# Kernel tuning notes

Measured on AMD Instinct MI355X. Metric: run time of the kernel, lower is better.

## Reference

```python
import jax, jax.numpy as jnp
import numpy as np

BIG = 1e6  # sentinel 'no zero pixel found yet' distance; BIG**2 = 1e12 fits fp32


def _edt(is_fg):
    """Exact Euclidean distance transform (scipy.distance_transform_edt semantics):
    distance from each nonzero pixel to the nearest zero pixel. is_fg: [N,H,W] bool.
    Separable exact algorithm: 1D vertical distance-to-zero per column via cummax
    scans, then min-plus convolution with the parabola (j-k)^2 along rows."""
    N, H, W = is_fg.shape
    is_zero = ~is_fg
    ih = jnp.arange(H, dtype=jnp.float32)[None, :, None]
    # nearest zero at-or-above / at-or-below along H (per column)
    up = jax.lax.cummax(jnp.where(is_zero, ih, -BIG), axis=1)
    dn = -jax.lax.cummax(jnp.where(is_zero, -ih, -BIG), axis=1, reverse=True)
    g = jnp.minimum(ih - up, dn - ih)               # [N,H,W] vertical 1D distance
    g2 = jnp.minimum(g, BIG) ** 2
    ks = jnp.arange(W, dtype=jnp.float32)
    def col(j):
        # exact 2D squared distance for output column j: min_k (j-k)^2 + g(.,.,k)^2
        return jnp.min((j.astype(jnp.float32) - ks) ** 2 + g2, axis=-1)  # [N,H]
    d2 = jax.lax.map(col, jnp.arange(W))            # [W,N,H], sequential -> low memory
    return jnp.sqrt(jnp.moveaxis(d2, 0, -1))        # [N,H,W]


def setup_inputs() -> dict:
    key = jax.random.key(0)
    k1, k2 = jax.random.split(key)
    B, C, H, W = 8, 12, 256, 256
    logits = jax.random.normal(k1, (B, C, H, W), dtype=jnp.float32)
    targets = jax.random.randint(k2, (B, H, W), 0, C, dtype=jnp.int32)
    return {"logits": logits, "targets": targets}


def reference(logits, targets):
    B, C, H, W = logits.shape
    probs = jax.nn.softmax(logits, axis=1)                                  # [B,C,H,W]
    gt = targets[:, None, :, :] == jnp.arange(C, dtype=targets.dtype)[None, :, None, None]
    m = gt.reshape(B * C, H, W)
    pos = _edt(m)          # distance inside foreground to nearest background
    neg = _edt(~m)         # distance inside background to nearest foreground
    dt = (neg - pos).reshape(B, C, H, W)
    has_fg = gt.any(axis=(2, 3))                                            # [B,C]
    dt = jnp.where(has_fg[:, :, None, None], dt, 0.0)
    # per-image, per-class min-max normalization (matches torch view(B,-1).min/max)
    dmin = dt.min(axis=(2, 3), keepdims=True)
    dmax = dt.max(axis=(2, 3), keepdims=True)
    dt = (dt - dmin) / (dmax - dmin + 1e-8)
    inter = jnp.sum(probs * dt, axis=(2, 3))                                # [B,C]
    denom = jnp.sum(probs * probs, axis=(2, 3)) + jnp.sum(dt * dt, axis=(2, 3)) + 1e-6
    dice = 2.0 * inter / denom
    # sum_c mean_b (1-dice) / C  == mean over (b,c) since ignore_index=255 is out of range
    return jnp.mean(1.0 - dice)
```

## Files before the change

kernel.cpp:

```cpp
#include <hip/hip_runtime.h>
#include <math.h>

constexpr int B_  = 8;
constexpr int C_  = 12;
constexpr int H_  = 256;
constexpr int W_  = 256;
constexpr int HW_ = H_ * W_;
constexpr int NBC_ = B_ * C_;
constexpr int PAD_ = 256;
constexpr int VB_  = NBC_ * 4;
constexpr int SMB_ = B_ * (HW_ / 1024);


__global__ void __launch_bounds__(256) k_vp(
                     const int* __restrict__ t,
                     const float* __restrict__ logits,
                     unsigned short* __restrict__ gpk,
                     int* __restrict__ hasfg_p,
                     float2* __restrict__ den,
                     float* __restrict__ out) {
    int tid = threadIdx.x;
    if (blockIdx.x >= VB_) {
        int pb = blockIdx.x - VB_;
        int b = pb >> 6;
        int p = ((pb & 63) << 10) + tid * 4;
        const float* lb = logits + (size_t)b * C_ * HW_ + p;
        float4 l[C_];
        float4 mx = make_float4(-3.4e38f, -3.4e38f, -3.4e38f, -3.4e38f);
        #pragma unroll
        for (int c = 0; c < C_; ++c) {
            l[c] = *(const float4*)(lb + (size_t)c * HW_);
            mx.x = fmaxf(mx.x, l[c].x);
            mx.y = fmaxf(mx.y, l[c].y);
            mx.z = fmaxf(mx.z, l[c].z);
            mx.w = fmaxf(mx.w, l[c].w);
        }
        float4 s = make_float4(0.f, 0.f, 0.f, 0.f);
        #pragma unroll
        for (int c = 0; c < C_; ++c) {
            s.x += __expf(l[c].x - mx.x);
            s.y += __expf(l[c].y - mx.y);
            s.z += __expf(l[c].z - mx.z);
            s.w += __expf(l[c].w - mx.w);
        }
        float2* dp = den + (size_t)b * HW_ + p;
        ((float4*)dp)[0] = make_float4(mx.x, 1.0f / s.x, mx.y, 1.0f / s.y);
        ((float4*)dp)[1] = make_float4(mx.z, 1.0f / s.z, mx.w, 1.0f / s.w);
        return;
    }

    if (blockIdx.x == 0 && tid == 0) out[0] = 0.0f;
    constexpr int SEG = 8, SH = 32;
    int s  = tid >> 5;
    int wl = tid & 31;
    int blk = blockIdx.x;
    int bc = blk >> 2;
    int w0 = (blk & 3) * 64;
    int b = bc / C_, c = bc - b * C_;
    int w = w0 + 2 * wl;
    const int* base = t + b * HW_ + w;
    int h0 = s * SH;

    unsigned tp0[SH / 4], tp1[SH / 4];
    int le0 = -1, ln0 = -1, fe0 = 256, fn0 = 256;
    int le1 = -1, ln1 = -1, fe1 = 256, fn1 = 256;
    #pragma unroll
    for (int i = 0; i < SH; ++i) {
        int2 tv = *(const int2*)(base + (h0 + i) * W_);
        if ((i & 3) == 0) { tp0[i >> 2] = 0; tp1[i >> 2] = 0; }
        tp0[i >> 2] |= (unsigned)tv.x << ((i & 3) * 8);
        tp1[i >> 2] |= (unsigned)tv.y << ((i & 3) * 8);
        int h = h0 + i;
        if (tv.x == c) { le0 = h; if (fe0 == 256) fe0 = h; }
        else           { ln0 = h; if (fn0 == 256) fn0 = h; }
        if (tv.y == c) { le1 = h; if (fe1 == 256) fe1 = h; }
        else           { ln1 = h; if (fn1 == 256) fn1 = h; }
    }
    __shared__ int sLE[SEG][64], sLN[SEG][64], sFE[SEG][64], sFN[SEG][64];
    sLE[s][2 * wl] = le0; sLE[s][2 * wl + 1] = le1;
    sLN[s][2 * wl] = ln0; sLN[s][2 * wl + 1] = ln1;
    sFE[s][2 * wl] = fe0; sFE[s][2 * wl + 1] = fe1;
    sFN[s][2 * wl] = fn0; sFN[s][2 * wl + 1] = fn1;
    __syncthreads();

    int carLE0 = -1, carLN0 = -1, carLE1 = -1, carLN1 = -1;
    for (int q = 0; q < s; ++q) {
        carLE0 = max(carLE0, sLE[q][2 * wl]);
        carLN0 = max(carLN0, sLN[q][2 * wl]);
        carLE1 = max(carLE1, sLE[q][2 * wl + 1]);
        carLN1 = max(carLN1, sLN[q][2 * wl + 1]);
    }
    int carFE0 = 256, carFN0 = 256, carFE1 = 256, carFN1 = 256;
    for (int q = s + 1; q < SEG; ++q) {
        carFE0 = min(carFE0, sFE[q][2 * wl]);
        carFN0 = min(carFN0, sFN[q][2 * wl]);
        carFE1 = min(carFE1, sFE[q][2 * wl + 1]);
        carFN1 = min(carFN1, sFN[q][2 * wl + 1]);
    }

    bool pred = false;
    if (tid < 64) {
        int m = -1;
        #pragma unroll
        for (int q = 0; q < SEG; ++q) m = max(m, sLE[q][tid]);
        pred = (m >= 0);
    }
    bool anyfg = __any(pred);
    if (tid == 0) hasfg_p[blk] = anyfg ? 1 : 0;

    unsigned ap0[SH / 4], ap1[SH / 4];
    {
        int l0 = carLE0, n0 = carLN0, l1 = carLE1, n1 = carLN1;
        #pragma unroll
        for (int i = 0; i < SH; ++i) {
            int h = h0 + i;
            int tv0 = (tp0[i >> 2] >> ((i & 3) * 8)) & 0xFF;
            int tv1 = (tp1[i >> 2] >> ((i & 3) * 8)) & 0xFF;
            int lz0, lz1;
            if (tv0 == c) { l0 = h; lz0 = n0; } else { n0 = h; lz0 = l0; }
            if (tv1 == c) { l1 = h; lz1 = n1; } else { n1 = h; lz1 = l1; }
            unsigned a0 = (lz0 < 0) ? 255u : (unsigned)(h - lz0 - 1);
            unsigned a1 = (lz1 < 0) ? 255u : (unsigned)(h - lz1 - 1);
            if ((i & 3) == 0) { ap0[i >> 2] = 0; ap1[i >> 2] = 0; }
            ap0[i >> 2] |= a0 << ((i & 3) * 8);
            ap1[i >> 2] |= a1 << ((i & 3) * 8);
        }
    }
    {
        int fe0_ = carFE0, fn0_ = carFN0, fe1_ = carFE1, fn1_ = carFN1;
        unsigned* gk32 = (unsigned*)(gpk + (size_t)bc * HW_ + w);
        #pragma unroll
        for (int i = SH - 1; i >= 0; --i) {
            int h = h0 + i;
            int tv0 = (tp0[i >> 2] >> ((i & 3) * 8)) & 0xFF;
            int tv1 = (tp1[i >> 2] >> ((i & 3) * 8)) & 0xFF;
            int nz0, nz1; bool fg0, fg1;
            if (tv0 == c) { fe0_ = h; fg0 = true;  nz0 = fn0_; }
            else          { fn0_ = h; fg0 = false; nz0 = fe0_; }
            if (tv1 == c) { fe1_ = h; fg1 = true;  nz1 = fn1_; }
            else          { fn1_ = h; fg1 = false; nz1 = fe1_; }
            unsigned au0 = (ap0[i >> 2] >> ((i & 3) * 8)) & 0xFF;
            unsigned au1 = (ap1[i >> 2] >> ((i & 3) * 8)) & 0xFF;
            int dl0 = (au0 == 255u) ? 0x7FFF : (int)au0 + 1;
            int dl1 = (au1 == 255u) ? 0x7FFF : (int)au1 + 1;
            int dn0 = (nz0 > 255) ? 0x7FFF : (nz0 - h);
            int dn1 = (nz1 > 255) ? 0x7FFF : (nz1 - h);
            unsigned d0 = (unsigned)min(dl0, dn0) | (fg0 ? 0x8000u : 0u);
            unsigned d1 = (unsigned)min(dl1, dn1) | (fg1 ? 0x8000u : 0u);
            gk32[(h * W_) >> 1] = d0 | (d1 << 16);
        }
    }
}

__global__ void __launch_bounds__(256) k_edt(
                      const unsigned short* __restrict__ gpk,
                      const float* __restrict__ logits,
                      const float2* __restrict__ den,
                      const int* __restrict__ hasfg_p,
                      float* __restrict__ part) {
    __shared__ float sp[4][W_ + 2 * PAD_];
    __shared__ float sn[4][W_ + 2 * PAD_];
    int wave = threadIdx.x >> 6;
    int lane = threadIdx.x & 63;
    int row = blockIdx.x * 4 + wave;
    int bc = row >> 8;
    int b = bc / C_, c = bc - b * C_;
    int h = row & (H_ - 1);

    int hfl = 0;
    if (lane < 4) hfl = hasfg_p[bc * 4 + lane];
    bool hf = __any(hfl != 0);

    const float*  lrow = logits + ((size_t)b * C_ + c) * HW_ + h * W_;
    const float2* drow = den + (size_t)b * HW_ + h * W_;
    float lv[4]; float2 mv[4];
    #pragma unroll
    for (int i = 0; i < 4; ++i) {
        int j = lane + 64 * i;
        lv[i] = lrow[j];
        mv[i] = drow[j];
    }

    float dv[4];
    if (hf) {
        const ushort4 v4 = ((const ushort4*)(gpk + (size_t)row * W_))[lane];

        float4 inf4 = make_float4(3.0e38f, 3.0e38f, 3.0e38f, 3.0e38f);
        ((float4*)&sp[wave][0])[lane]          = inf4;
        ((float4*)&sp[wave][PAD_ + W_])[lane]  = inf4;
        ((float4*)&sn[wave][0])[lane]          = inf4;
        ((float4*)&sn[wave][PAD_ + W_])[lane]  = inf4;

        float s1 = (float)(1000000 - h);
        float sent2 = s1 * s1;
        float4 fpv, fnv;
        {
            const unsigned short* vs = (const unsigned short*)&v4;
            float* fp = (float*)&fpv;
            float* fn = (float*)&fnv;
            #pragma unroll
            for (int q = 0; q < 4; ++q) {
                unsigned v = vs[q];
                unsigned d = v & 0x7FFFu;
                float g2 = (d == 0x7FFFu) ? sent2 : (float)(d * d);
                bool fg = (v & 0x8000u) != 0;
                fp[q] = fg ? g2 : 0.0f;
                fn[q] = fg ? 0.0f : g2;
            }
        }
        ((float4*)&sp[wave][PAD_])[lane] = fpv;
        ((float4*)&sn[wave][PAD_])[lane] = fnv;
        asm volatile("s_waitcnt lgkmcnt(0)" ::: "memory");

        float bp[4], bn[4];
        #pragma unroll
        for (int i = 0; i < 4; ++i) {
            int j = PAD_ + lane + 64 * i;
            bp[i] = sp[wave][j];
            bn[i] = sn[wave][j];
        }
        for (int r = 1; r < W_; ++r) {
            float fr = (float)r;
            float r2 = fr * fr;
            float m = fmaxf(fmaxf(bn[0], bn[1]), fmaxf(bn[2], bn[3]));
            if (!__any(r2 < m)) break;
            #pragma unroll
            for (int i = 0; i < 4; ++i) {
                int j = PAD_ + lane + 64 * i;
                float v = fminf(sn[wave][j - r], sn[wave][j + r]);
                bn[i] = fminf(bn[i], fmaf(fr, fr, v));
            }
        }
        for (int r = 1; r < W_; ++r) {
            float fr = (float)r;
            float r2 = fr * fr;
            float m = fmaxf(fmaxf(bp[0], bp[1]), fmaxf(bp[2], bp[3]));
            if (!__any(r2 < m)) break;
            #pragma unroll
            for (int i = 0; i < 4; ++i) {
                int j = PAD_ + lane + 64 * i;
                float v = fminf(sp[wave][j - r], sp[wave][j + r]);
                bp[i] = fminf(bp[i], fmaf(fr, fr, v));
            }
        }
        #pragma unroll
        for (int i = 0; i < 4; ++i) dv[i] = sqrtf(bn[i]) - sqrtf(bp[i]);
    } else {
        #pragma unroll
        for (int i = 0; i < 4; ++i) dv[i] = 0.0f;
    }

    float s_pd = 0.f, s_p = 0.f, s_pp = 0.f, s_d = 0.f, s_dd = 0.f;
    float mn = 3.4e38f, mx = -3.4e38f;
    #pragma unroll
    for (int i = 0; i < 4; ++i) {
        float2 mi = mv[i];
        float pr = __expf(lv[i] - mi.x) * mi.y;
        float d = dv[i];
        s_pd = fmaf(pr, d, s_pd);
        s_p += pr;
        s_pp = fmaf(pr, pr, s_pp);
        s_d += d;
        s_dd = fmaf(d, d, s_dd);
        mn = fminf(mn, d);
        mx = fmaxf(mx, d);
    }
    #pragma unroll
    for (int off = 32; off; off >>= 1) {
        s_pd += __shfl_down(s_pd, off);
        s_p  += __shfl_down(s_p, off);
        s_pp += __shfl_down(s_pp, off);
        s_d  += __shfl_down(s_d, off);
        s_dd += __shfl_down(s_dd, off);
        mn = fminf(mn, __shfl_down(mn, off));
        mx = fmaxf(mx, __shfl_down(mx, off));
    }
    if (lane == 0) {
        float* p8 = part + (size_t)row * 8;
        p8[0] = s_pd; p8[1] = s_p; p8[2] = s_pp;
        p8[3] = s_d;  p8[4] = s_dd; p8[5] = mn; p8[6] = mx;
    }
}

__global__ void __launch_bounds__(256) k_bcred(
                       const float* __restrict__ part, float* __restrict__ out) {
    int bc = blockIdx.x;
    int tid = threadIdx.x;
    const float* p8 = part + ((size_t)bc * 256 + tid) * 8;
    float s_pd = p8[0], s_p = p8[1], s_pp = p8[2];
    float s_d = p8[3], s_dd = p8[4], mn = p8[5], mx = p8[6];
    #pragma unroll
    for (int off = 32; off; off >>= 1) {
        s_pd += __shfl_down(s_pd, off);
        s_p  += __shfl_down(s_p, off);
        s_pp += __shfl_down(s_pp, off);
        s_d  += __shfl_down(s_d, off);
        s_dd += __shfl_down(s_dd, off);
        mn = fminf(mn, __shfl_down(mn, off));
        mx = fmaxf(mx, __shfl_down(mx, off));
    }
    __shared__ float red[4][7];
    int wave = tid >> 6, lane = tid & 63;
    if (lane == 0) {
        red[wave][0] = s_pd; red[wave][1] = s_p; red[wave][2] = s_pp;
        red[wave][3] = s_d;  red[wave][4] = s_dd; red[wave][5] = mn; red[wave][6] = mx;
    }
    __syncthreads();
    if (tid == 0) {
        s_pd = red[0][0]; s_p = red[0][1]; s_pp = red[0][2];
        s_d = red[0][3]; s_dd = red[0][4]; mn = red[0][5]; mx = red[0][6];
        for (int w = 1; w < 4; ++w) {
            s_pd += red[w][0]; s_p += red[w][1]; s_pp += red[w][2];
            s_d += red[w][3]; s_dd += red[w][4];
            mn = fminf(mn, red[w][5]); mx = fmaxf(mx, red[w][6]);
        }
        float sc = 1.0f / (mx - mn + 1e-8f);
        float inter = sc * (s_pd - mn * s_p);
        float d2 = sc * sc * (s_dd - 2.0f * mn * s_d + mn * mn * (float)HW_);
        float dice = 2.0f * inter / (s_pp + d2 + 1e-6f);
        atomicAdd(out, (1.0f - dice) * (1.0f / (float)NBC_));
    }
}

extern "C" void kernel_launch(void* const* d_in, const int* in_sizes, int n_in,
                              void* d_out, int out_size, void* d_ws, size_t ws_size,
                              hipStream_t stream) {
    const float* logits  = (const float*)d_in[0];
    const int*   targets = (const int*)d_in[1];
    float* out = (float*)d_out;

    unsigned short* gpk = (unsigned short*)d_ws;
    int* hasfg_p = (int*)(gpk + (size_t)NBC_ * HW_);
    float* part = (float*)(hasfg_p + NBC_ * 8);
    float2* den = (float2*)(part + (size_t)NBC_ * H_ * 8);

    k_vp<<<VB_ + SMB_, 256, 0, stream>>>(targets, logits, gpk,
                                         hasfg_p, den, out);
    k_edt<<<NBC_ * H_ / 4, 256, 0, stream>>>(gpk, logits, den, hasfg_p, part);
    k_bcred<<<NBC_, 256, 0, stream>>>(part, out);
}
```

Baseline: 109.7 us.

## Fuse softmax stats into EDT kernel, one block per image row across classes

```diff
diff --git a/kernel.cpp b/kernel.cpp
--- a/kernel.cpp
+++ b/kernel.cpp
@@ -9,46 +9,15 @@
 constexpr int NBC_ = B_ * C_;
 constexpr int PAD_ = 256;
 constexpr int VB_  = NBC_ * 4;
-constexpr int SMB_ = B_ * (HW_ / 1024);
+constexpr int E2B_ = B_ * H_;
 
 
 __global__ void __launch_bounds__(256) k_vp(
                      const int* __restrict__ t,
-                     const float* __restrict__ logits,
                      unsigned short* __restrict__ gpk,
                      int* __restrict__ hasfg_p,
-                     float2* __restrict__ den,
                      float* __restrict__ out) {
     int tid = threadIdx.x;
-    if (blockIdx.x >= VB_) {
-        int pb = blockIdx.x - VB_;
-        int b = pb >> 6;
-        int p = ((pb & 63) << 10) + tid * 4;
-        const float* lb = logits + (size_t)b * C_ * HW_ + p;
-        float4 l[C_];
-        float4 mx = make_float4(-3.4e38f, -3.4e38f, -3.4e38f, -3.4e38f);
-        #pragma unroll
-        for (int c = 0; c < C_; ++c) {
-            l[c] = *(const float4*)(lb + (size_t)c * HW_);
-            mx.x = fmaxf(mx.x, l[c].x);
-            mx.y = fmaxf(mx.y, l[c].y);
-            mx.z = fmaxf(mx.z, l[c].z);
-            mx.w = fmaxf(mx.w, l[c].w);
-        }
-        float4 s = make_float4(0.f, 0.f, 0.f, 0.f);
-        #pragma unroll
-        for (int c = 0; c < C_; ++c) {
-            s.x += __expf(l[c].x - mx.x);
-            s.y += __expf(l[c].y - mx.y);
-            s.z += __expf(l[c].z - mx.z);
-            s.w += __expf(l[c].w - mx.w);
-        }
-        float2* dp = den + (size_t)b * HW_ + p;
-        ((float4*)dp)[0] = make_float4(mx.x, 1.0f / s.x, mx.y, 1.0f / s.y);
-        ((float4*)dp)[1] = make_float4(mx.z, 1.0f / s.z, mx.w, 1.0f / s.w);
-        return;
-    }
-
     if (blockIdx.x == 0 && tid == 0) out[0] = 0.0f;
     constexpr int SEG = 8, SH = 32;
     int s  = tid >> 5;
@@ -152,119 +121,165 @@
     }
 }
 
-__global__ void __launch_bounds__(256) k_edt(
+__global__ void __launch_bounds__(256) k_edt2(
                       const unsigned short* __restrict__ gpk,
                       const float* __restrict__ logits,
-                      const float2* __restrict__ den,
                       const int* __restrict__ hasfg_p,
                       float* __restrict__ part) {
     __shared__ float sp[4][W_ + 2 * PAD_];
     __shared__ float sn[4][W_ + 2 * PAD_];
-    int wave = threadIdx.x >> 6;
-    int lane = threadIdx.x & 63;
-    int row = blockIdx.x * 4 + wave;
-    int bc = row >> 8;
-    int b = bc / C_, c = bc - b * C_;
-    int h = row & (H_ - 1);
-
-    int hfl = 0;
-    if (lane < 4) hfl = hasfg_p[bc * 4 + lane];
-    bool hf = __any(hfl != 0);
-
-    const float*  lrow = logits + ((size_t)b * C_ + c) * HW_ + h * W_;
-    const float2* drow = den + (size_t)b * HW_ + h * W_;
-    float lv[4]; float2 mv[4];
-    #pragma unroll
-    for (int i = 0; i < 4; ++i) {
-        int j = lane + 64 * i;
-        lv[i] = lrow[j];
-        mv[i] = drow[j];
-    }
-
-    float dv[4];
-    if (hf) {
-        const ushort4 v4 = ((const ushort4*)(gpk + (size_t)row * W_))[lane];
-
-        float4 inf4 = make_float4(3.0e38f, 3.0e38f, 3.0e38f, 3.0e38f);
-        ((float4*)&sp[wave][0])[lane]          = inf4;
-        ((float4*)&sp[wave][PAD_ + W_])[lane]  = inf4;
-        ((float4*)&sn[wave][0])[lane]          = inf4;
-        ((float4*)&sn[wave][PAD_ + W_])[lane]  = inf4;
-
-        float s1 = (float)(1000000 - h);
-        float sent2 = s1 * s1;
-        float4 fpv, fnv;
-        {
-            const unsigned short* vs = (const unsigned short*)&v4;
-            float* fp = (float*)&fpv;
-            float* fn = (float*)&fnv;
-            #pragma unroll
-            for (int q = 0; q < 4; ++q) {
-                unsigned v = vs[q];
-                unsigned d = v & 0x7FFFu;
-                float g2 = (d == 0x7FFFu) ? sent2 : (float)(d * d);
-                bool fg = (v & 0x8000u) != 0;
-                fp[q] = fg ? g2 : 0.0f;
-                fn[q] = fg ? 0.0f : g2;
+    int tid  = threadIdx.x;
+    int wave = tid >> 6;
+    int lane = tid & 63;
+    int blk = blockIdx.x;
+    int b = blk >> 8;
+    int h = blk & (H_ - 1);
+
+    float4 inf4 = make_float4(3.0e38f, 3.0e38f, 3.0e38f, 3.0e38f);
+    ((float4*)&sp[wave][0])[lane]          = inf4;
+    ((float4*)&sp[wave][PAD_ + W_])[lane]  = inf4;
+    ((float4*)&sn[wave][0])[lane]          = inf4;
+    ((float4*)&sn[wave][PAD_ + W_])[lane]  = inf4;
+
+    const float* lb = logits + (size_t)b * C_ * HW_ + h * W_;
+    float mx4[4] = {-3.4e38f, -3.4e38f, -3.4e38f, -3.4e38f};
+    #pragma unroll
+    for (int c = 0; c < C_; ++c) {
+        #pragma unroll
+        for (int i = 0; i < 4; ++i)
+            mx4[i] = fmaxf(mx4[i], lb[(size_t)c * HW_ + lane + 64 * i]);
+    }
+    float s4[4] = {0.f, 0.f, 0.f, 0.f};
+    #pragma unroll
+    for (int c = 0; c < C_; ++c) {
+        #pragma unroll
+        for (int i = 0; i < 4; ++i)
+            s4[i] += __expf(lb[(size_t)c * HW_ + lane + 64 * i] - mx4[i]);
+    }
+    float inv4[4];
+    #pragma unroll
+    for (int i = 0; i < 4; ++i) inv4[i] = 1.0f / s4[i];
+
+    int c0 = wave * 3;
+    float l3[3][4];
+    #pragma unroll
+    for (int q = 0; q < 3; ++q)
+        #pragma unroll
+        for (int i = 0; i < 4; ++i)
+            l3[q][i] = lb[(size_t)(c0 + q) * HW_ + lane + 64 * i];
+
+    float s1 = (float)(1000000 - h);
+    float sent2 = s1 * s1;
+
+    #pragma unroll
+    for (int q = 0; q < 3; ++q) {
+        int c = c0 + q;
+        int bc = b * C_ + c;
+        int row = bc * H_ + h;
+
+        int hfl = 0;
+        if (lane < 4) hfl = hasfg_p[bc * 4 + lane];
+        bool hf = __any(hfl != 0);
+
+        float dv[4];
+        if (hf) {
+            const ushort4 v4 = ((const ushort4*)(gpk + (size_t)bc * HW_ + h * W_))[lane];
+            float4 fpv, fnv;
+            {
+                const unsigned short* vs = (const unsigned short*)&v4;
+                float* fp = (float*)&fpv;
+                float* fn = (float*)&fnv;
+                #pragma unroll
+                for (int k2 = 0; k2 < 4; ++k2) {
+                    unsigned v = vs[k2];
+                    unsigned d = v & 0x7FFFu;
+                    float g2 = (d == 0x7FFFu) ? sent2 : (float)(d * d);
+                    bool fg = (v & 0x8000u) != 0;
+                    fp[k2] = fg ? g2 : 0.0f;
+                    fn[k2] = fg ? 0.0f : g2;
+                }
             }
-        }
-        ((float4*)&sp[wave][PAD_])[lane] = fpv;
-        ((float4*)&sn[wave][PAD_])[lane] = fnv;
-        asm volatile("s_waitcnt lgkmcnt(0)" ::: "memory");
-
-        float bp[4], bn[4];
-        #pragma unroll
-        for (int i = 0; i < 4; ++i) {
-            int j = PAD_ + lane + 64 * i;
-            bp[i] = sp[wave][j];
-            bn[i] = sn[wave][j];
-        }
-        for (int r = 1; r < W_; ++r) {
-            float fr = (float)r;
-            float r2 = fr * fr;
-            float m = fmaxf(fmaxf(bn[0], bn[1]), fmaxf(bn[2], bn[3]));
-            if (!__any(r2 < m)) break;
+            ((float4*)&sp[wave][PAD_])[lane] = fpv;
+            ((float4*)&sn[wave][PAD_])[lane] = fnv;
+            asm volatile("s_waitcnt lgkmcnt(0)" ::: "memory");
+
+            float bp[4], bn[4];
             #pragma unroll
             for (int i = 0; i < 4; ++i) {
                 int j = PAD_ + lane + 64 * i;
-                float v = fminf(sn[wave][j - r], sn[wave][j + r]);
-                bn[i] = fminf(bn[i], fmaf(fr, fr, v));
+                bp[i] = sp[wave][j];
+                bn[i] = sn[wave][j];
             }
-        }
-        for (int r = 1; r < W_; ++r) {
-            float fr = (float)r;
-            float r2 = fr * fr;
-            float m = fmaxf(fmaxf(bp[0], bp[1]), fmaxf(bp[2], bp[3]));
-            if (!__any(r2 < m)) break;
+            for (int r = 1; r < W_; ++r) {
+                float fr = (float)r;
+                float r2 = fr * fr;
+                float m = fmaxf(fmaxf(bn[0], bn[1]), fmaxf(bn[2], bn[3]));
+                if (!__any(r2 < m)) break;
+                #pragma unroll
+                for (int i = 0; i < 4; ++i) {
+                    int j = PAD_ + lane + 64 * i;
+                    float v = fminf(sn[wave][j - r], sn[wave][j + r]);
+                    bn[i] = fminf(bn[i], fmaf(fr, fr, v));
+                }
+            }
+            for (int r = 1; r < W_; ++r) {
+                float fr = (float)r;
+                float r2 = fr * fr;
+                float m = fmaxf(fmaxf(bp[0], bp[1]), fmaxf(bp[2], bp[3]));
+                if (!__any(r2 < m)) break;
+                #pragma unroll
+                for (int i = 0; i < 4; ++i) {
+                    int j = PAD_ + lane + 64 * i;
+                    float v = fminf(sp[wave][j - r], sp[wave][j + r]);
+                    bp[i] = fminf(bp[i], fmaf(fr, fr, v));
+                }
+            }
             #pragma unroll
-            for (int i = 0; i < 4; ++i) {
-                int j = PAD_ + lane + 64 * i;
-                float v = fminf(sp[wave][j - r], sp[wave][j + r]);
-                bp[i] = fminf(bp[i], fmaf(fr, fr, v));
-            }
-        }
-        #pragma unroll
-        for (int i = 0; i < 4; ++i) dv[i] = sqrtf(bn[i]) - sqrtf(bp[i]);
-    } else {
-        #pragma unroll
-        for (int i = 0; i < 4; ++i) dv[i] = 0.0f;
-    }
-
-    float s_pd = 0.f, s_p = 0.f, s_pp = 0.f, s_d = 0.f, s_dd = 0.f;
-    float mn = 3.4e38f, mx = -3.4e38f;
-    #pragma unroll
-    for (int i = 0; i < 4; ++i) {
-        float2 mi = mv[i];
-        float pr = __expf(lv[i] - mi.x) * mi.y;
-        float d = dv[i];
-        s_pd = fmaf(pr, d, s_pd);
-        s_p += pr;
-        s_pp = fmaf(pr, pr, s_pp);
-        s_d += d;
-        s_dd = fmaf(d, d, s_dd);
-        mn = fminf(mn, d);
-        mx = fmaxf(mx, d);
-    }
+            for (int i = 0; i < 4; ++i) dv[i] = sqrtf(bn[i]) - sqrtf(bp[i]);
+        } else {
+            #pragma unroll
+            for (int i = 0; i < 4; ++i) dv[i] = 0.0f;
+        }
+
+        float s_pd = 0.f, s_p = 0.f, s_pp = 0.f, s_d = 0.f, s_dd = 0.f;
+        float mn = 3.4e38f, mx = -3.4e38f;
+        #pragma unroll
+        for (int i = 0; i < 4; ++i) {
+            float pr = __expf(l3[q][i] - mx4[i]) * inv4[i];
+            float d = dv[i];
+            s_pd = fmaf(pr, d, s_pd);
+            s_p += pr;
+            s_pp = fmaf(pr, pr, s_pp);
+            s_d += d;
+            s_dd = fmaf(d, d, s_dd);
+            mn = fminf(mn, d);
+            mx = fmaxf(mx, d);
+        }
+        #pragma unroll
+        for (int off = 32; off; off >>= 1) {
+            s_pd += __shfl_down(s_pd, off);
+            s_p  += __shfl_down(s_p, off);
+            s_pp += __shfl_down(s_pp, off);
+            s_d  += __shfl_down(s_d, off);
+            s_dd += __shfl_down(s_dd, off);
+            mn = fminf(mn, __shfl_down(mn, off));
+            mx = fmaxf(mx, __shfl_down(mx, off));
+        }
+        if (lane == 0) {
+            float* p8 = part + (size_t)row * 8;
+            p8[0] = s_pd; p8[1] = s_p; p8[2] = s_pp;
+            p8[3] = s_d;  p8[4] = s_dd; p8[5] = mn; p8[6] = mx;
+        }
+    }
+}
+
+__global__ void __launch_bounds__(256) k_bcred(
+                       const float* __restrict__ part, float* __restrict__ out) {
+    int bc = blockIdx.x;
+    int tid = threadIdx.x;
+    const float* p8 = part + ((size_t)bc * 256 + tid) * 8;
+    float s_pd = p8[0], s_p = p8[1], s_pp = p8[2];
+    float s_d = p8[3], s_dd = p8[4], mn = p8[5], mx = p8[6];
     #pragma unroll
     for (int off = 32; off; off >>= 1) {
         s_pd += __shfl_down(s_pd, off);
@@ -275,30 +290,6 @@
         mn = fminf(mn, __shfl_down(mn, off));
         mx = fmaxf(mx, __shfl_down(mx, off));
     }
-    if (lane == 0) {
-        float* p8 = part + (size_t)row * 8;
-        p8[0] = s_pd; p8[1] = s_p; p8[2] = s_pp;
-        p8[3] = s_d;  p8[4] = s_dd; p8[5] = mn; p8[6] = mx;
-    }
-}
-
-__global__ void __launch_bounds__(256) k_bcred(
-                       const float* __restrict__ part, float* __restrict__ out) {
-    int bc = blockIdx.x;
-    int tid = threadIdx.x;
-    const float* p8 = part + ((size_t)bc * 256 + tid) * 8;
-    float s_pd = p8[0], s_p = p8[1], s_pp = p8[2];
-    float s_d = p8[3], s_dd = p8[4], mn = p8[5], mx = p8[6];
-    #pragma unroll
-    for (int off = 32; off; off >>= 1) {
-        s_pd += __shfl_down(s_pd, off);
-        s_p  += __shfl_down(s_p, off);
-        s_pp += __shfl_down(s_pp, off);
-        s_d  += __shfl_down(s_d, off);
-        s_dd += __shfl_down(s_dd, off);
-        mn = fminf(mn, __shfl_down(mn, off));
-        mx = fmaxf(mx, __shfl_down(mx, off));
-    }
     __shared__ float red[4][7];
     int wave = tid >> 6, lane = tid & 63;
     if (lane == 0) {
@@ -331,11 +322,9 @@
 
     unsigned short* gpk = (unsigned short*)d_ws;
     int* hasfg_p = (int*)(gpk + (size_t)NBC_ * HW_);
-    float* part = (float*)(hasfg_p + NBC_ * 8);
-    float2* den = (float2*)(part + (size_t)NBC_ * H_ * 8);
-
-    k_vp<<<VB_ + SMB_, 256, 0, stream>>>(targets, logits, gpk,
-                                         hasfg_p, den, out);
-    k_edt<<<NBC_ * H_ / 4, 256, 0, stream>>>(gpk, logits, den, hasfg_p, part);
+    float* part = (float*)(hasfg_p + VB_);
+
+    k_vp<<<VB_, 256, 0, stream>>>(targets, gpk, hasfg_p, out);
+    k_edt2<<<E2B_, 256, 0, stream>>>(gpk, logits, hasfg_p, part);
     k_bcred<<<NBC_, 256, 0, stream>>>(part, out);
 }
```

Result: slower. 115.9 us (+5.6%).
